# Performance work log

Measured on AMD Instinct MI355X. Metric: run time of the kernel, lower is better.

## Reference

```python
import jax, jax.numpy as jnp
import numpy as np

B, S, D, FF, E, K = 4, 2048, 1024, 4096, 16, 2
EPS = 1e-6
MOE_SCALING = 1.0


def setup_inputs() -> dict:
    key = jax.random.key(0)
    k0, k1, k2, k3 = jax.random.split(key, 4)
    hidden_states = jax.random.normal(k0, (B, S, D), jnp.float32)
    ln_weight = jnp.ones((D,), jnp.float32)
    gate_w = jax.random.normal(k1, (D, E), jnp.float32) * 0.02
    gate_b = jnp.zeros((E,), jnp.float32)
    wi = jax.random.normal(k2, (E, D, FF), jnp.float32) * (1.0 / np.sqrt(D).astype(np.float32))
    wo = jax.random.normal(k3, (E, FF, D), jnp.float32) * (1.0 / np.sqrt(FF).astype(np.float32))
    return {"hidden_states": hidden_states, "ln_weight": ln_weight,
            "gate_w": gate_w, "gate_b": gate_b, "wi": wi, "wo": wo}


def reference(hidden_states, ln_weight, gate_w, gate_b, wi, wo):
    # --- T5LayerNorm (RMS norm, no mean subtraction, no bias) ---
    var = jnp.mean(hidden_states * hidden_states, axis=-1, keepdims=True)
    norm_x = hidden_states * jax.lax.rsqrt(var + EPS) * ln_weight

    T = B * S
    xt = norm_x.reshape(T, D)  # tokens

    # --- NaiveGate: linear -> top-k -> softmax over selected logits ---
    logits = xt @ gate_w + gate_b                      # [T, E]
    top_vals, top_idx = jax.lax.top_k(logits, K)       # [T, K]
    scores = jax.nn.softmax(top_vals, axis=-1)         # [T, K]
    # dense combine weights [T, E] (zero for non-selected experts)
    combine = jnp.zeros((T, E), xt.dtype).at[jnp.arange(T)[:, None], top_idx].add(scores)

    # --- expert FFNs (T5DenseReluDense per expert), combined by gate weight ---
    def body(acc, xs):
        w_i, w_o, c = xs                               # [D,FF], [FF,D], [T]
        h = jax.nn.relu(xt @ w_i)                      # [T, FF]
        return acc + c[:, None] * (h @ w_o), None

    y0 = jnp.zeros((T, D), xt.dtype)
    y, _ = jax.lax.scan(body, y0, (wi, wo, combine.T))

    y = MOE_SCALING * y
    # dropout is identity at eval; scaled residual add
    layer_output = hidden_states + y.reshape(B, S, D)
    return layer_output
```

## Files before the change

kernel.cpp:

```cpp
#include <hip/hip_runtime.h>

#define T_TOK 8192
#define DIM   1024
#define FFD   4096
#define NEXP  16

typedef __bf16 bf16_t;
typedef bf16_t bf16x4 __attribute__((ext_vector_type(4)));
typedef bf16_t bf16x8 __attribute__((ext_vector_type(8)));
typedef float  f32x4  __attribute__((ext_vector_type(4)));

__device__ __forceinline__ void gload_lds16(const void* g, void* l) {
  __builtin_amdgcn_global_load_lds((__attribute__((address_space(1))) void*)(g),
                                   (__attribute__((address_space(3))) void*)(l),
                                   16, 0, 0);
}

__global__ __launch_bounds__(256) void k_norm_gate(
    const float* __restrict__ x, const float* __restrict__ lnw,
    const float* __restrict__ gw, const float* __restrict__ gb,
    bf16_t* __restrict__ xt, int* __restrict__ cnt,
    int* __restrict__ stok, float* __restrict__ swgt,
    int* __restrict__ tslot)
{
  const int t = blockIdx.x;
  const int tid = threadIdx.x;
  const int wave = tid >> 6, lane = tid & 63;

  float4 v = ((const float4*)(x + (size_t)t * DIM))[tid];
  float ss = v.x*v.x + v.y*v.y + v.z*v.z + v.w*v.w;
  #pragma unroll
  for (int off = 32; off > 0; off >>= 1) ss += __shfl_down(ss, off, 64);

  __shared__ float red[4];
  __shared__ float racc[4][16];
  if (lane == 0) red[wave] = ss;
  __syncthreads();
  float r = rsqrtf((red[0]+red[1]+red[2]+red[3]) * (1.0f/DIM) + 1e-6f);

  float4 lw = ((const float4*)lnw)[tid];
  float nv[4];
  nv[0] = v.x*r*lw.x; nv[1] = v.y*r*lw.y; nv[2] = v.z*r*lw.z; nv[3] = v.w*r*lw.w;
  bf16x4 nb; nb[0]=(bf16_t)nv[0]; nb[1]=(bf16_t)nv[1]; nb[2]=(bf16_t)nv[2]; nb[3]=(bf16_t)nv[3];
  ((bf16x4*)(xt + (size_t)t * DIM))[tid] = nb;

  float acc[16];
  #pragma unroll
  for (int e=0;e<16;e++) acc[e]=0.f;
  #pragma unroll
  for (int j=0;j<4;j++){
    const float4* row = (const float4*)(gw + ((size_t)(tid*4+j))*16);
    #pragma unroll
    for (int q=0;q<4;q++){
      float4 g = row[q];
      acc[q*4+0] += nv[j]*g.x;
      acc[q*4+1] += nv[j]*g.y;
      acc[q*4+2] += nv[j]*g.z;
      acc[q*4+3] += nv[j]*g.w;
    }
  }
  #pragma unroll
  for (int e=0;e<16;e++){
    #pragma unroll
    for (int off=32;off>0;off>>=1) acc[e] += __shfl_down(acc[e], off, 64);
  }
  if (lane==0){
    #pragma unroll
    for (int e=0;e<16;e++) racc[wave][e]=acc[e];
  }
  __syncthreads();
  if (tid==0){
    float lg[16];
    #pragma unroll
    for (int e=0;e<16;e++) lg[e] = racc[0][e]+racc[1][e]+racc[2][e]+racc[3][e] + gb[e];
    int i0=0; float v0=lg[0];
    for (int e=1;e<16;e++) if (lg[e]>v0){v0=lg[e]; i0=e;}
    int i1=-1; float v1=-3.4e38f;
    for (int e=0;e<16;e++) if (e!=i0 && lg[e]>v1){v1=lg[e]; i1=e;}
    float ex = expf(v1-v0);
    float s0 = 1.0f/(1.0f+ex);
    float s1 = ex * s0;
    int p0 = atomicAdd(&cnt[i0],1);
    stok[i0*T_TOK+p0]=t; swgt[i0*T_TOK+p0]=s0;
    int p1 = atomicAdd(&cnt[i1],1);
    stok[i1*T_TOK+p1]=t; swgt[i1*T_TOK+p1]=s1;
    tslot[2*t+0] = (i0<<16) | p0;
    tslot[2*t+1] = (i1<<16) | p1;
  }
}

__global__ void k_offsets(const int* __restrict__ cnt, int* __restrict__ offs){
  if (threadIdx.x==0){
    int s=0;
    for (int e=0;e<NEXP;e++){ offs[e]=s; s+=cnt[e]; }
    offs[NEXP]=s;
  }
}

__global__ __launch_bounds__(256) void k_transpose(
    const float* __restrict__ in, bf16_t* __restrict__ out, int R, int C)
{
  __shared__ float tile[64][68];
  const int e = blockIdx.z;
  const int r0 = blockIdx.y*64, c0 = blockIdx.x*64;
  const int tr = threadIdx.x >> 4, tc4 = (threadIdx.x & 15)*4;
  const float* src = in + ((size_t)e*R + r0)*C + c0;
  #pragma unroll
  for (int i=0;i<4;i++){
    int rr = tr + i*16;
    float4 vv = *(const float4*)(src + (size_t)rr*C + tc4);
    tile[rr][tc4+0]=vv.x; tile[rr][tc4+1]=vv.y; tile[rr][tc4+2]=vv.z; tile[rr][tc4+3]=vv.w;
  }
  __syncthreads();
  bf16_t* dst = out + ((size_t)e*C + c0)*R + r0;
  #pragma unroll
  for (int i=0;i<4;i++){
    int cc = tr + i*16;
    bf16x4 b;
    b[0]=(bf16_t)tile[tc4+0][cc];
    b[1]=(bf16_t)tile[tc4+1][cc];
    b[2]=(bf16_t)tile[tc4+2][cc];
    b[3]=(bf16_t)tile[tc4+3][cc];
    *(bf16x4*)(dst + (size_t)cc*R + tc4) = b;
  }
}

template<int KD, bool G1>
__global__ __launch_bounds__(256) void k_gemm(
    const bf16_t* __restrict__ A0, const bf16_t* __restrict__ Bt,
    const int* __restrict__ cnt, const int* __restrict__ offs,
    const int* __restrict__ stok, const float* __restrict__ swgt,
    bf16_t* __restrict__ Hout, float* __restrict__ Out)
{
  const int e  = blockIdx.z;
  const int cn = cnt[e];
  const int m0 = blockIdx.y * 128;
  if (m0 >= cn) return;
  const int n0 = blockIdx.x * 128;
  const int oe = offs[e];
  constexpr int NR = G1 ? FFD : DIM;

  __shared__ bf16_t As[128*64];
  __shared__ bf16_t Bs[128*64];

  const int tid  = threadIdx.x;
  const int wave = tid >> 6, lane = tid & 63;
  const int lrow = lane >> 3;
  const int lcol = (((lane & 7) ^ lrow) * 8);

  const bf16_t* aptr[4];
  const bf16_t* bptr[4];
  #pragma unroll
  for (int j=0;j<4;j++){
    int chunk = wave*4 + j;
    int r = chunk*8 + lrow;
    int grow = m0 + r;
    if constexpr (G1){
      int tok = (grow < cn) ? stok[e*T_TOK + grow] : 0;
      aptr[j] = A0 + (size_t)tok*KD + lcol;
    } else {
      aptr[j] = A0 + (size_t)(oe + grow)*KD + lcol;
    }
    bptr[j] = Bt + ((size_t)e*NR + (n0 + r))*KD + lcol;
  }

  f32x4 acc[4][4];
  #pragma unroll
  for (int mt=0;mt<4;mt++)
    #pragma unroll
    for (int nt=0;nt<4;nt++)
      #pragma unroll
      for (int q=0;q<4;q++) acc[mt][nt][q]=0.f;

  const int wm = wave & 1, wn = wave >> 1;
  const bf16_t* aslds = As + ((wm*64) + (lane & 15))*64;
  const bf16_t* bslds = Bs + ((wn*64) + (lane & 15))*64;
  const int swz0 = ((((lane>>4) + 0) ^ (lane & 7)) * 8);
  const int swz1 = ((((lane>>4) + 4) ^ (lane & 7)) * 8);

  for (int k0=0; k0<KD; k0+=64){
    #pragma unroll
    for (int j=0;j<4;j++){
      gload_lds16(aptr[j] + k0, As + (wave*4+j)*512);
      gload_lds16(bptr[j] + k0, Bs + (wave*4+j)*512);
    }
    __syncthreads();
    #pragma unroll
    for (int kc=0;kc<64;kc+=32){
      const int swz = (kc == 0) ? swz0 : swz1;
      bf16x8 af[4], bfr[4];
      #pragma unroll
      for (int mt=0;mt<4;mt++) af[mt]  = *(const bf16x8*)(aslds + mt*1024 + swz);
      #pragma unroll
      for (int nt=0;nt<4;nt++) bfr[nt] = *(const bf16x8*)(bslds + nt*1024 + swz);
      #pragma unroll
      for (int mt=0;mt<4;mt++)
        #pragma unroll
        for (int nt=0;nt<4;nt++)
          acc[mt][nt] = __builtin_amdgcn_mfma_f32_16x16x32_bf16(af[mt], bfr[nt], acc[mt][nt], 0, 0, 0);
    }
    __syncthreads();
  }

  const int lq = lane >> 4;
  const int lc = lane & 15;
  #pragma unroll
  for (int mt=0;mt<4;mt++){
    #pragma unroll
    for (int i=0;i<4;i++){
      int rl = wm*64 + mt*16 + lq*4 + i;
      int grow = m0 + rl;
      if (grow < cn){
        if constexpr (G1){
          float w = swgt[e*T_TOK + grow];
          size_t hbase = (size_t)(oe + grow) * FFD;
          #pragma unroll
          for (int nt=0;nt<4;nt++){
            int colg = n0 + wn*64 + nt*16 + lc;
            float vv = acc[mt][nt][i];
            vv = vv > 0.f ? vv * w : 0.f;
            Hout[hbase + colg] = (bf16_t)vv;
          }
        } else {
          size_t obase = (size_t)(oe + grow) * DIM;
          #pragma unroll
          for (int nt=0;nt<4;nt++){
            int colg = n0 + wn*64 + nt*16 + lc;
            Out[obase + colg] = acc[mt][nt][i];
          }
        }
      }
    }
  }
}

__global__ __launch_bounds__(256) void k_combine(
    const float* __restrict__ hidden, const float* __restrict__ y2,
    const int* __restrict__ offs, const int* __restrict__ tslot,
    float* __restrict__ out)
{
  const int t = blockIdx.x;
  const int tid = threadIdx.x;
  const int s0 = tslot[2*t+0], s1 = tslot[2*t+1];
  const size_t r0 = (size_t)(offs[s0>>16] + (s0 & 0xffff));
  const size_t r1 = (size_t)(offs[s1>>16] + (s1 & 0xffff));
  float4 a = ((const float4*)(hidden + (size_t)t*DIM))[tid];
  float4 b = ((const float4*)(y2 + r0*DIM))[tid];
  float4 c = ((const float4*)(y2 + r1*DIM))[tid];
  a.x += b.x + c.x;
  a.y += b.y + c.y;
  a.z += b.z + c.z;
  a.w += b.w + c.w;
  ((float4*)(out + (size_t)t*DIM))[tid] = a;
}

extern "C" void kernel_launch(void* const* d_in, const int* in_sizes, int n_in,
                              void* d_out, int out_size, void* d_ws, size_t ws_size,
                              hipStream_t stream) {
  const float* hidden = (const float*)d_in[0];
  const float* lnw    = (const float*)d_in[1];
  const float* gw     = (const float*)d_in[2];
  const float* gb     = (const float*)d_in[3];
  const float* wi     = (const float*)d_in[4];
  const float* wo     = (const float*)d_in[5];
  float* out = (float*)d_out;

  char* ws = (char*)d_ws;
  size_t o = 0;
  auto alloc = [&](size_t bytes)->char*{ char* p = ws + o; o += (bytes + 255) & ~(size_t)255; return p; };
  bf16_t* xt   = (bf16_t*)alloc((size_t)T_TOK*DIM*2);
  bf16_t* wiT  = (bf16_t*)alloc((size_t)NEXP*FFD*DIM*2);
  bf16_t* woT  = (bf16_t*)alloc((size_t)NEXP*DIM*FFD*2);
  bf16_t* h    = (bf16_t*)alloc((size_t)(2*T_TOK + 128)*FFD*2);
  int*    stok = (int*)alloc((size_t)NEXP*T_TOK*4);
  float*  swgt = (float*)alloc((size_t)NEXP*T_TOK*4);
  int*    tslot= (int*)alloc((size_t)2*T_TOK*4);
  int*    cnt  = (int*)alloc(256);
  int*    offs = (int*)alloc(256);
  (void)ws_size; (void)in_sizes; (void)n_in; (void)out_size;

  float* y2 = (float*)wiT;

  hipMemsetAsync(cnt, 0, 64, stream);

  k_norm_gate<<<dim3(T_TOK), 256, 0, stream>>>(hidden, lnw, gw, gb, xt, cnt, stok, swgt, tslot);
  k_offsets<<<dim3(1), 64, 0, stream>>>(cnt, offs);
  k_transpose<<<dim3(FFD/64, DIM/64, NEXP), 256, 0, stream>>>(wi, wiT, DIM, FFD);
  k_transpose<<<dim3(DIM/64, FFD/64, NEXP), 256, 0, stream>>>(wo, woT, FFD, DIM);
  k_gemm<DIM, true ><<<dim3(FFD/128, T_TOK/128, NEXP), 256, 0, stream>>>(xt, wiT, cnt, offs, stok, swgt, h, nullptr);
  k_gemm<FFD, false><<<dim3(DIM/128, T_TOK/128, NEXP), 256, 0, stream>>>(h,  woT, cnt, offs, stok, swgt, nullptr, y2);
  k_combine<<<dim3(T_TOK), 256, 0, stream>>>(hidden, y2, offs, tslot, out);
}
```

Baseline: 1.309 ms.

## Merge weight transposes into one bf16 swizzled-LDS kernel and parallelize gate atomics

Both weight transposes now run in a single launch. Each block converts fp32 to bf16 before staging it in a half-size, XOR-swizzled LDS tile, then writes 16-byte bf16x8 rows instead of 8-byte ones. The gate's two atomic scatters now run in two parallel threads instead of serially in thread 0, at the cost of an extra block barrier. The aim is to cut launch overhead, LDS traffic and bank conflicts, and to widen global stores in the weight-conversion pass, which moves about 512MB of fp32 weights on every call.

```diff
diff --git a/kernel.cpp b/kernel.cpp
--- a/kernel.cpp
+++ b/kernel.cpp
@@ -34,6 +34,8 @@
 
   __shared__ float red[4];
   __shared__ float racc[4][16];
+  __shared__ int   sel[2];
+  __shared__ float swv[2];
   if (lane == 0) red[wave] = ss;
   __syncthreads();
   float r = rsqrtf((red[0]+red[1]+red[2]+red[3]) * (1.0f/DIM) + 1e-6f);
@@ -80,12 +82,14 @@
     float ex = expf(v1-v0);
     float s0 = 1.0f/(1.0f+ex);
     float s1 = ex * s0;
-    int p0 = atomicAdd(&cnt[i0],1);
-    stok[i0*T_TOK+p0]=t; swgt[i0*T_TOK+p0]=s0;
-    int p1 = atomicAdd(&cnt[i1],1);
-    stok[i1*T_TOK+p1]=t; swgt[i1*T_TOK+p1]=s1;
-    tslot[2*t+0] = (i0<<16) | p0;
-    tslot[2*t+1] = (i1<<16) | p1;
+    sel[0]=i0; sel[1]=i1; swv[0]=s0; swv[1]=s1;
+  }
+  __syncthreads();
+  if (tid<2){
+    int ii = sel[tid]; float sv = swv[tid];
+    int p = atomicAdd(&cnt[ii],1);
+    stok[ii*T_TOK+p]=t; swgt[ii*T_TOK+p]=sv;
+    tslot[2*t+tid] = (ii<<16) | p;
   }
 }
 
@@ -97,31 +101,46 @@
   }
 }
 
-__global__ __launch_bounds__(256) void k_transpose(
-    const float* __restrict__ in, bf16_t* __restrict__ out, int R, int C)
+__global__ __launch_bounds__(256) void k_transpose2(
+    const float* __restrict__ wi, bf16_t* __restrict__ wiT,
+    const float* __restrict__ wo, bf16_t* __restrict__ woT)
 {
-  __shared__ float tile[64][68];
-  const int e = blockIdx.z;
-  const int r0 = blockIdx.y*64, c0 = blockIdx.x*64;
-  const int tr = threadIdx.x >> 4, tc4 = (threadIdx.x & 15)*4;
-  const float* src = in + ((size_t)e*R + r0)*C + c0;
-  #pragma unroll
-  for (int i=0;i<4;i++){
-    int rr = tr + i*16;
-    float4 vv = *(const float4*)(src + (size_t)rr*C + tc4);
-    tile[rr][tc4+0]=vv.x; tile[rr][tc4+1]=vv.y; tile[rr][tc4+2]=vv.z; tile[rr][tc4+3]=vv.w;
+  __shared__ bf16_t lds[64*64];
+  const int z = blockIdx.z;
+  const float* in; bf16_t* out; int R, C, bx, by, e;
+  if (z < NEXP){ in=wi; out=wiT; R=DIM; C=FFD; e=z;
+                 bx=blockIdx.x; by=blockIdx.y; }
+  else        { in=wo; out=woT; R=FFD; C=DIM; e=z-NEXP;
+                 bx=blockIdx.x & 15; by=blockIdx.y + 16*(blockIdx.x>>4); }
+  const int r0 = by*64, c0 = bx*64;
+  const int tid = threadIdx.x;
+
+  {
+    const int rr = tid >> 4;
+    const int c4 = (tid & 15) * 4;
+    const float* src = in + ((size_t)e*R + r0 + rr)*C + c0 + c4;
+    #pragma unroll
+    for (int i=0;i<4;i++){
+      int rrow = rr + i*16;
+      float4 vv = *(const float4*)(src + (size_t)i*16*C);
+      bf16x4 b; b[0]=(bf16_t)vv.x; b[1]=(bf16_t)vv.y; b[2]=(bf16_t)vv.z; b[3]=(bf16_t)vv.w;
+      int swz = ((rrow >> 3) & 7) << 3;
+      *(bf16x4*)(lds + rrow*64 + (c4 ^ swz)) = b;
+    }
   }
   __syncthreads();
-  bf16_t* dst = out + ((size_t)e*C + c0)*R + r0;
-  #pragma unroll
-  for (int i=0;i<4;i++){
-    int cc = tr + i*16;
-    bf16x4 b;
-    b[0]=(bf16_t)tile[tc4+0][cc];
-    b[1]=(bf16_t)tile[tc4+1][cc];
-    b[2]=(bf16_t)tile[tc4+2][cc];
-    b[3]=(bf16_t)tile[tc4+3][cc];
-    *(bf16x4*)(dst + (size_t)cc*R + tc4) = b;
+  {
+    const int r8  = (tid & 7) * 8;
+    const int cc  = tid >> 3;
+    const int swz = (tid & 7) << 3;
+    #pragma unroll
+    for (int i=0;i<2;i++){
+      int c = cc + i*32;
+      bf16x8 b;
+      #pragma unroll
+      for (int j=0;j<8;j++) b[j] = lds[(r8+j)*64 + (c ^ swz)];
+      *(bf16x8*)(out + ((size_t)e*C + c0 + c)*R + r0 + r8) = b;
+    }
   }
 }
 
@@ -285,8 +304,7 @@
 
   k_norm_gate<<<dim3(T_TOK), 256, 0, stream>>>(hidden, lnw, gw, gb, xt, cnt, stok, swgt, tslot);
   k_offsets<<<dim3(1), 64, 0, stream>>>(cnt, offs);
-  k_transpose<<<dim3(FFD/64, DIM/64, NEXP), 256, 0, stream>>>(wi, wiT, DIM, FFD);
-  k_transpose<<<dim3(DIM/64, FFD/64, NEXP), 256, 0, stream>>>(wo, woT, FFD, DIM);
+  k_transpose2<<<dim3(64, 16, 2*NEXP), 256, 0, stream>>>(wi, wiT, wo, woT);
   k_gemm<DIM, true ><<<dim3(FFD/128, T_TOK/128, NEXP), 256, 0, stream>>>(xt, wiT, cnt, offs, stok, swgt, h, nullptr);
   k_gemm<FFD, false><<<dim3(DIM/128, T_TOK/128, NEXP), 256, 0, stream>>>(h,  woT, cnt, offs, stok, swgt, nullptr, y2);
   k_combine<<<dim3(T_TOK), 256, 0, stream>>>(hidden, y2, offs, tslot, out);
```

Measured after the change: 1.212 ms. 1.08x faster.
